# Performance work log

Hardware: AMD Instinct MI355X
Metric: run time of the kernel (lower is better)

The kernel has to match this reference:

```python
import jax, jax.numpy as jnp
import numpy as np

T, B, V, E = 256, 128, 256, 512
NN = (1024, 1024)  # num_nodes per LSTM layer


def setup_inputs() -> dict:
    key = jax.random.key(0)
    ks = jax.random.split(key, 8)
    inputs = jax.random.normal(ks[0], (T, B, V), jnp.float32)
    emb = jax.random.normal(ks[1], (V, E), jnp.float32) * np.float32(np.sqrt(1.0 / V))
    w0 = jax.random.normal(ks[2], (E + NN[0], 4 * NN[0]), jnp.float32) * np.float32(np.sqrt(1.0 / (E + NN[0])))
    b0 = jnp.zeros((4 * NN[0],), jnp.float32)
    w1 = jax.random.normal(ks[3], (NN[0] + NN[1], 4 * NN[1]), jnp.float32) * np.float32(np.sqrt(1.0 / (NN[0] + NN[1])))
    b1 = jnp.zeros((4 * NN[1],), jnp.float32)
    out_w = jax.random.normal(ks[4], (NN[1], V), jnp.float32) * np.float32(np.sqrt(1.0 / NN[1]))
    out_b = jnp.zeros((V,), jnp.float32)
    return {"inputs": inputs, "embedding_matrix": emb,
            "lstm_w0": w0, "lstm_b0": b0, "lstm_w1": w1, "lstm_b1": b1,
            "out_w": out_w, "out_b": out_b}


def reference(inputs, embedding_matrix, lstm_w0, lstm_b0, lstm_w1, lstm_b1, out_w, out_b):
    Tn, Bn, _ = inputs.shape
    # _embed: (stacked one-hot) @ embedding_matrix -> [T, B, E]
    embs = jnp.einsum('tbv,ve->tbe', inputs, embedding_matrix)
    ws = (lstm_w0, lstm_w1)
    bs = (lstm_b0, lstm_b1)
    init_states = tuple((jnp.zeros((Bn, n), embs.dtype), jnp.zeros((Bn, n), embs.dtype)) for n in NN)

    def step(states, emb):
        out = emb
        new_states = []
        for i in range(len(NN)):
            h, c = states[i]
            n = NN[i]
            # concat([dropout(inp), h]) @ W + b ; dropout_keep_prob = 1.0 -> identity
            lin = jnp.concatenate([out, h], axis=1) @ ws[i] + bs[i]
            f = jax.nn.sigmoid(lin[:, :n])
            ig = jax.nn.sigmoid(lin[:, n:2 * n])
            o = jax.nn.sigmoid(lin[:, 2 * n:3 * n])
            g = jnp.tanh(lin[:, 3 * n:])
            c = f * c + ig * g
            h = o * jnp.tanh(c)
            out = h
            new_states.append((h, c))
        return tuple(new_states), out

    _, rnn_outputs = jax.lax.scan(step, init_states, embs)  # [T, B, NN[-1]]
    # output module: concat over time (axis 0) then single dense layer
    hs = rnn_outputs.reshape(Tn * Bn, NN[-1])
    logits = hs @ out_w + out_b  # [T*B, V]
    return logits
```

## Files before the change

kernel.cpp:

```cpp
#include <hip/hip_runtime.h>
#include <hip/hip_bf16.h>
#include <cstdint>
#include <cstddef>

#define T_STEPS 256
#define BATCH   128
#define VOCAB   256
#define EDIM    512
#define NH      1024
#define GDIM    4096
#define NST0    40
#define NST1    64

typedef __attribute__((ext_vector_type(8))) short short8;
typedef __attribute__((ext_vector_type(4))) float floatx4;

__device__ __forceinline__ float sigmoidf_(float x) { return 1.0f / (1.0f + __expf(-x)); }
__device__ __forceinline__ float tanhf_(float x)    { return 1.0f - 2.0f / (__expf(2.0f * x) + 1.0f); }

typedef __attribute__((address_space(1))) const unsigned int guint;
typedef __attribute__((address_space(3))) unsigned int luint;
__device__ __forceinline__ void load_lds16(const void* g, void* l) {
    __builtin_amdgcn_global_load_lds((guint*)g, (luint*)l, 16, 0, 0);
}

#define BM 128
#define BN 128
#define BK 16
__global__ __launch_bounds__(256) void sgemm_f32(
    const float* __restrict__ A, const float* __restrict__ B,
    float* __restrict__ C, int M, int N, int K)
{
    __shared__ float As[BK][BM + 4];
    __shared__ float Bs[BK][BN + 4];
    const int tid = threadIdx.x;
    const int tr = tid >> 4, tc = tid & 15;
    const int bm = blockIdx.y, bn = blockIdx.x;
    const float* Ab = A + (size_t)bm * BM * K;
    float acc[8][8];
    #pragma unroll
    for (int i = 0; i < 8; ++i)
        #pragma unroll
        for (int j = 0; j < 8; ++j) acc[i][j] = 0.f;
    for (int k0 = 0; k0 < K; k0 += BK) {
        #pragma unroll
        for (int l = 0; l < 2; ++l) {
            int idx = tid + l * 256;
            int row = idx >> 2, c4 = idx & 3;
            float4 v = *(const float4*)(Ab + (size_t)row * K + k0 + c4 * 4);
            As[c4 * 4 + 0][row] = v.x; As[c4 * 4 + 1][row] = v.y;
            As[c4 * 4 + 2][row] = v.z; As[c4 * 4 + 3][row] = v.w;
        }
        #pragma unroll
        for (int l = 0; l < 2; ++l) {
            int idx = tid + l * 256;
            int row = idx >> 5, c4 = idx & 31;
            *(float4*)&Bs[row][c4 * 4] = *(const float4*)(B + (size_t)(k0 + row) * N + bn * BN + c4 * 4);
        }
        __syncthreads();
        #pragma unroll
        for (int kk = 0; kk < BK; ++kk) {
            float4 a0 = *(const float4*)&As[kk][tr * 8];
            float4 a1 = *(const float4*)&As[kk][tr * 8 + 4];
            float4 b0 = *(const float4*)&Bs[kk][tc * 8];
            float4 b1 = *(const float4*)&Bs[kk][tc * 8 + 4];
            float av[8] = {a0.x, a0.y, a0.z, a0.w, a1.x, a1.y, a1.z, a1.w};
            float bv[8] = {b0.x, b0.y, b0.z, b0.w, b1.x, b1.y, b1.z, b1.w};
            #pragma unroll
            for (int i = 0; i < 8; ++i)
                #pragma unroll
                for (int j = 0; j < 8; ++j) acc[i][j] += av[i] * bv[j];
        }
        __syncthreads();
    }
    #pragma unroll
    for (int i = 0; i < 8; ++i) {
        size_t row = (size_t)bm * BM + tr * 8 + i;
        #pragma unroll
        for (int j = 0; j < 8; j += 4) {
            int col = bn * BN + tc * 8 + j;
            *(float4*)(C + row * N + col) =
                make_float4(acc[i][j], acc[i][j+1], acc[i][j+2], acc[i][j+3]);
        }
    }
}

__global__ __launch_bounds__(256) void transpose_to_bf16(
    const float* __restrict__ src, __hip_bfloat16* __restrict__ dst, int R, int C)
{
    __shared__ float t[32][33];
    int x = blockIdx.x * 32 + threadIdx.x;
    #pragma unroll
    for (int i = 0; i < 4; ++i) {
        int y = blockIdx.y * 32 + threadIdx.y + i * 8;
        t[threadIdx.y + i * 8][threadIdx.x] = src[(size_t)y * C + x];
    }
    __syncthreads();
    int x2 = blockIdx.y * 32 + threadIdx.x;
    #pragma unroll
    for (int i = 0; i < 4; ++i) {
        int y2 = blockIdx.x * 32 + threadIdx.y + i * 8;
        dst[(size_t)y2 * R + x2] = __float2bfloat16(t[threadIdx.x][threadIdx.y + i * 8]);
    }
}

__global__ __launch_bounds__(256) void pack_w2(
    const float* __restrict__ src, __hip_bfloat16* __restrict__ dst,
    int koff, int NSTEPS)
{
    __shared__ float t[64][33];
    const int tid = threadIdx.x;
    const int xt = blockIdx.x;
    const int kt = blockIdx.y;
    {
        int yl = tid >> 3;
        int x0 = (tid & 7) * 8;
        const float* p = src + (size_t)(kt * 32 + yl) * GDIM + xt * 64 + x0;
        float4 v0 = *(const float4*)p;
        float4 v1 = *(const float4*)(p + 4);
        t[x0 + 0][yl] = v0.x; t[x0 + 1][yl] = v0.y; t[x0 + 2][yl] = v0.z; t[x0 + 3][yl] = v0.w;
        t[x0 + 4][yl] = v1.x; t[x0 + 5][yl] = v1.y; t[x0 + 6][yl] = v1.z; t[x0 + 7][yl] = v1.w;
    }
    __syncthreads();
    {
        int ll = tid >> 2;
        int quad = tid & 3;
        int lincol = xt * 64 + ll;
        int g = lincol >> 10, n = lincol & 1023;
        int j = n >> 3, c = n & 7;
        int tt = g >> 1;
        int l16 = (g & 1) * 8 + c;
        int s = (koff >> 5) + kt;
        __hip_bfloat16 o[8];
        #pragma unroll
        for (int jj = 0; jj < 8; ++jj)
            o[jj] = __float2bfloat16(t[ll][quad * 8 + jj]);
        size_t off = ((((size_t)j * NSTEPS + s) * 2 + tt) * 64 + (size_t)quad * 16 + l16) * 8;
        *(uint4*)(dst + off) = *(const uint4*)o;
    }
}

__global__ __launch_bounds__(256) void convert_to_bf16(
    const float* __restrict__ src, __hip_bfloat16* __restrict__ dst, size_t n4)
{
    size_t i = (size_t)blockIdx.x * 256 + threadIdx.x;
    if (i < n4) {
        float4 v = *(const float4*)(src + i * 4);
        __hip_bfloat16 o[4] = {__float2bfloat16(v.x), __float2bfloat16(v.y),
                               __float2bfloat16(v.z), __float2bfloat16(v.w)};
        *(uint2*)(dst + i * 4) = *(uint2*)o;
    }
}

#define GKP 40
__global__ __launch_bounds__(256) void gemm_bt(
    const __hip_bfloat16* __restrict__ A, const __hip_bfloat16* __restrict__ Bt,
    const float* __restrict__ bias, float* __restrict__ C, int M, int N, int K)
{
    __shared__ __hip_bfloat16 As[128 * GKP];
    __shared__ __hip_bfloat16 Bs[128 * GKP];
    const int tid = threadIdx.x;
    const int wave = tid >> 6, lane = tid & 63;
    const int quad = lane >> 4, l16 = lane & 15;
    const int wm = (wave >> 1) * 64, wn = (wave & 1) * 64;
    const size_t Arow0 = (size_t)blockIdx.y * 128;
    const size_t Brow0 = (size_t)blockIdx.x * 128;
    floatx4 acc[4][4];
    #pragma unroll
    for (int i = 0; i < 4; ++i)
        #pragma unroll
        for (int j = 0; j < 4; ++j) acc[i][j] = (floatx4)0.f;

    for (int k0 = 0; k0 < K; k0 += 32) {
        #pragma unroll
        for (int l = 0; l < 2; ++l) {
            int idx = tid + l * 256;
            int row = idx >> 2, seg = idx & 3;
            *(uint4*)(As + row * GKP + seg * 8) =
                *(const uint4*)(A + (Arow0 + row) * K + k0 + seg * 8);
            *(uint4*)(Bs + row * GKP + seg * 8) =
                *(const uint4*)(Bt + (Brow0 + row) * K + k0 + seg * 8);
        }
        __syncthreads();
        short8 af[4], bf[4];
        #pragma unroll
        for (int i = 0; i < 4; ++i)
            af[i] = *(const short8*)(As + (wm + i * 16 + l16) * GKP + quad * 8);
        #pragma unroll
        for (int j = 0; j < 4; ++j)
            bf[j] = *(const short8*)(Bs + (wn + j * 16 + l16) * GKP + quad * 8);
        #pragma unroll
        for (int i = 0; i < 4; ++i)
            #pragma unroll
            for (int j = 0; j < 4; ++j)
                acc[i][j] = __builtin_amdgcn_mfma_f32_16x16x32_bf16(af[i], bf[j], acc[i][j], 0, 0, 0);
        __syncthreads();
    }
    #pragma unroll
    for (int i = 0; i < 4; ++i)
        #pragma unroll
        for (int j = 0; j < 4; ++j) {
            int col = (int)Brow0 + wn + j * 16 + l16;
            float bv = bias ? bias[col] : 0.f;
            #pragma unroll
            for (int r = 0; r < 4; ++r) {
                size_t row = Arow0 + wm + i * 16 + quad * 4 + r;
                C[row * N + col] = acc[i][j][r] + bv;
            }
        }
}

template<int NC, int NCA0>
__device__ __forceinline__ void lstm_chunks(
    const __hip_bfloat16* __restrict__ pA0,
    const __hip_bfloat16* __restrict__ pA1,
    const __hip_bfloat16* Wlds, int lane,
    floatx4& acc0, floatx4& acc1)
{
    constexpr int D = 3;
    constexpr int P = (NC < D) ? NC : D;
    short8 af[D][8];
    #pragma unroll
    for (int c = 0; c < P; ++c) {
        const __hip_bfloat16* pa = (c < NCA0) ? (pA0 + (size_t)c * 256)
                                              : (pA1 + (size_t)(c - NCA0) * 256);
        #pragma unroll
        for (int ss = 0; ss < 8; ++ss)
            af[c % D][ss] = *(const short8*)(pa + ss * 32);
    }
    __syncthreads();
    #pragma unroll
    for (int c = 0; c < NC; ++c) {
        #pragma unroll
        for (int ss = 0; ss < 8; ++ss) {
            const int s = c * 8 + ss;
            short8 bf0 = *(const short8*)&Wlds[s * 1024 + lane * 8];
            short8 bf1 = *(const short8*)&Wlds[s * 1024 + 512 + lane * 8];
            acc0 = __builtin_amdgcn_mfma_f32_16x16x32_bf16(af[c % D][ss], bf0, acc0, 0, 0, 0);
            acc1 = __builtin_amdgcn_mfma_f32_16x16x32_bf16(af[c % D][ss], bf1, acc1, 0, 0, 0);
        }
        if (c + D < NC) {
            const int cn = c + D;
            const __hip_bfloat16* pa = (cn < NCA0) ? (pA0 + (size_t)cn * 256)
                                                   : (pA1 + (size_t)(cn - NCA0) * 256);
            #pragma unroll
            for (int ss = 0; ss < 8; ++ss)
                af[cn % D][ss] = *(const short8*)(pa + ss * 32);
        }
    }
}

__global__ __launch_bounds__(512) void lstm_diag(
    const __hip_bfloat16* __restrict__ inbf,
    const __hip_bfloat16* __restrict__ Wpack0,
    const __hip_bfloat16* __restrict__ Wpack1,
    const float* __restrict__ b0, const float* __restrict__ b1,
    __hip_bfloat16* __restrict__ h0_cur,
    const __hip_bfloat16* __restrict__ h0_prev,
    float* __restrict__ c0, float* __restrict__ c1,
    __hip_bfloat16* __restrict__ H1all,
    int d)
{
    const int bid = blockIdx.x;
    const int layer = (bid >> 3) & 1;
    const int j = ((bid >> 4) << 3) | (bid & 7);
    if (layer == 0 && d >= T_STEPS) return;
    if (layer == 1 && d == 0) return;

    __shared__ __attribute__((aligned(16))) __hip_bfloat16 Wlds[65536];

    const int tid = threadIdx.x;
    const int wave = tid >> 6, lane = tid & 63;
    const int quad = lane >> 4, l16 = lane & 15;

    const __hip_bfloat16 *A0, *A1;
    int A0stride;
    const float* bb; float* cst; __hip_bfloat16* hout;
    bool first;
    if (layer == 0) {
        first = (d == 0);
        bb = b0; cst = c0;
        A0 = inbf + (size_t)d * (BATCH * VOCAB); A0stride = VOCAB;
        A1 = h0_prev;
        hout = h0_cur;
        const __hip_bfloat16* Wp = Wpack0 + (size_t)j * (NST0 * 1024);
        #pragma unroll
        for (int it = 0; it < 10; ++it)
            load_lds16(Wp + it * 4096 + tid * 8, Wlds + it * 4096 + tid * 8);
    } else {
        first = (d == 1);
        bb = b1; cst = c1;
        A0 = h0_prev; A0stride = NH;
        A1 = (d >= 2) ? (H1all + (size_t)(d - 2) * (BATCH * NH)) : h0_prev;
        hout = H1all + (size_t)(d - 1) * (BATCH * NH);
        const __hip_bfloat16* Wp = Wpack1 + (size_t)j * (NST1 * 1024);
        #pragma unroll
        for (int it = 0; it < 16; ++it)
            load_lds16(Wp + it * 4096 + tid * 8, Wlds + it * 4096 + tid * 8);
    }

    const int row = wave * 16 + l16;
    const __hip_bfloat16* pA0 = A0 + (size_t)row * A0stride + quad * 8;
    const __hip_bfloat16* pA1 = A1 + (size_t)row * NH + quad * 8;

    const int cc = j * 8 + (l16 & 7);
    float bv0 = bb[((l16 < 8) ? 0 : 1) * NH + cc];
    float bv1 = bb[((l16 < 8) ? 2 : 3) * NH + cc];
    float cold[4];
    {
        const int bbase = 16 * wave + quad * 4;
        #pragma unroll
        for (int r = 0; r < 4; ++r)
            cold[r] = first ? 0.f : cst[(size_t)(bbase + r) * NH + cc];
    }
    floatx4 acc0 = {bv0, bv0, bv0, bv0};
    floatx4 acc1 = {bv1, bv1, bv1, bv1};

    if (layer == 0) {
        if (first) lstm_chunks<1, 1>(pA0, pA1, Wlds, lane, acc0, acc1);
        else       lstm_chunks<5, 1>(pA0, pA1, Wlds, lane, acc0, acc1);
    } else {
        if (first) lstm_chunks<4, 4>(pA0, pA1, Wlds, lane, acc0, acc1);
        else       lstm_chunks<8, 4>(pA0, pA1, Wlds, lane, acc0, acc1);
    }

    #pragma unroll
    for (int r = 0; r < 4; ++r) {
        float a0 = acc0[r], a1 = acc1[r];
        float p0 = __shfl_xor(a0, 8, 64);
        float p1 = __shfl_xor(a1, 8, 64);
        if (l16 < 8) {
            int b = 16 * wave + quad * 4 + r;
            float f  = sigmoidf_(a0);
            float ig = sigmoidf_(p0);
            float oo = sigmoidf_(a1);
            float gg = tanhf_(p1);
            size_t idx = (size_t)b * NH + cc;
            float cn = f * cold[r] + ig * gg;
            float hn = oo * tanhf_(cn);
            cst[idx] = cn;
            hout[idx] = __float2bfloat16(hn);
        }
    }
}

extern "C" void kernel_launch(void* const* d_in, const int* in_sizes, int n_in,
                              void* d_out, int out_size, void* d_ws, size_t ws_size,
                              hipStream_t stream)
{
    const float* inputs = (const float*)d_in[0];
    const float* emb    = (const float*)d_in[1];
    const float* w0     = (const float*)d_in[2];
    const float* b0     = (const float*)d_in[3];
    const float* w1     = (const float*)d_in[4];
    const float* b1     = (const float*)d_in[5];
    const float* outw   = (const float*)d_in[6];
    const float* outb   = (const float*)d_in[7];
    float* out = (float*)d_out;

    char* ws = (char*)d_ws;
    size_t off = 0;
    auto take = [&](size_t bytes) { char* p = ws + off; off += (bytes + 255) & ~(size_t)255; return p; };
    float* Wcomb = (float*)take((size_t)VOCAB * GDIM * 4);
    __hip_bfloat16* Wpack0 = (__hip_bfloat16*)take((size_t)128 * NST0 * 1024 * 2);
    __hip_bfloat16* Wpack1 = (__hip_bfloat16*)take((size_t)128 * NST1 * 1024 * 2);
    __hip_bfloat16* outwt  = (__hip_bfloat16*)take((size_t)NH * VOCAB * 2);
    __hip_bfloat16* inbf   = (__hip_bfloat16*)take((size_t)T_STEPS * BATCH * VOCAB * 2);
    __hip_bfloat16* h0pp0  = (__hip_bfloat16*)take((size_t)BATCH * NH * 2);
    __hip_bfloat16* h0pp1  = (__hip_bfloat16*)take((size_t)BATCH * NH * 2);
    float* c0 = (float*)take((size_t)BATCH * NH * 4);
    float* c1 = (float*)take((size_t)BATCH * NH * 4);
    __hip_bfloat16* H1all  = (__hip_bfloat16*)take((size_t)T_STEPS * BATCH * NH * 2);

    sgemm_f32<<<dim3(GDIM / BN, VOCAB / BM), 256, 0, stream>>>(
        emb, w0, Wcomb, VOCAB, GDIM, EDIM);
    pack_w2<<<dim3(64, VOCAB / 32), 256, 0, stream>>>(Wcomb, Wpack0, 0, NST0);
    pack_w2<<<dim3(64, NH / 32), 256, 0, stream>>>(w0 + (size_t)EDIM * GDIM, Wpack0, VOCAB, NST0);
    pack_w2<<<dim3(64, NH / 32), 256, 0, stream>>>(w1, Wpack1, 0, NST1);
    pack_w2<<<dim3(64, NH / 32), 256, 0, stream>>>(w1 + (size_t)NH * GDIM, Wpack1, NH, NST1);
    transpose_to_bf16<<<dim3(VOCAB / 32, NH / 32), dim3(32, 8), 0, stream>>>(
        outw, outwt, NH, VOCAB);
    {
        size_t n4 = (size_t)T_STEPS * BATCH * VOCAB / 4;
        convert_to_bf16<<<(int)((n4 + 255) / 256), 256, 0, stream>>>(inputs, inbf, n4);
    }

    for (int d = 0; d <= T_STEPS; ++d) {
        __hip_bfloat16* hcur = (d & 1) ? h0pp1 : h0pp0;
        __hip_bfloat16* hprev = (d & 1) ? h0pp0 : h0pp1;
        lstm_diag<<<256, 512, 0, stream>>>(
            inbf, Wpack0, Wpack1, b0, b1, hcur, hprev, c0, c1, H1all, d);
    }

    gemm_bt<<<dim3(VOCAB / 128, (T_STEPS * BATCH) / 128), 256, 0, stream>>>(
        H1all, outwt, outb, out, T_STEPS * BATCH, VOCAB, NH);
}
```

Measured before the change: 5.857 ms.

## Replace per-step LSTM launches with persistent cooperative kernel using grid barriers

Replaces the 257 per-diagonal kernel launches with one cooperative persistent kernel. It loads each block's packed weight slice into LDS once and keeps the cell state in registers. Steps are separated by an atomic-counter grid barrier, and the operand order is reordered so the shared h0 chunks are consumed with matching weight chunk offsets. This removes launch overhead, the repeated weight reloads into LDS and the cell-state global traffic. The cost is a grid-wide spin barrier per step and a dependence on all 256 blocks being co-resident, with a fallback to the old loop if the cooperative launch fails.

```diff
diff --git a/kernel.cpp b/kernel.cpp
--- a/kernel.cpp
+++ b/kernel.cpp
@@ -210,30 +210,30 @@
         }
 }
 
-template<int NC, int NCA0>
-__device__ __forceinline__ void lstm_chunks(
-    const __hip_bfloat16* __restrict__ pA0,
-    const __hip_bfloat16* __restrict__ pA1,
+template<int NCF, int NCS, int WF, int WS>
+__device__ __forceinline__ void chunks2(
+    const __hip_bfloat16* __restrict__ pF,
+    const __hip_bfloat16* __restrict__ pS,
     const __hip_bfloat16* Wlds, int lane,
     floatx4& acc0, floatx4& acc1)
 {
-    constexpr int D = 3;
-    constexpr int P = (NC < D) ? NC : D;
-    short8 af[D][8];
-    #pragma unroll
-    for (int c = 0; c < P; ++c) {
-        const __hip_bfloat16* pa = (c < NCA0) ? (pA0 + (size_t)c * 256)
-                                              : (pA1 + (size_t)(c - NCA0) * 256);
+    constexpr int NC = NCF + NCS;
+    constexpr int D = (NC < 3) ? NC : 3;
+    short8 af[3][8];
+    #pragma unroll
+    for (int c = 0; c < D; ++c) {
+        const __hip_bfloat16* pa = (c < NCF) ? (pF + (size_t)c * 256)
+                                             : (pS + (size_t)(c - NCF) * 256);
         #pragma unroll
         for (int ss = 0; ss < 8; ++ss)
             af[c % D][ss] = *(const short8*)(pa + ss * 32);
     }
-    __syncthreads();
     #pragma unroll
     for (int c = 0; c < NC; ++c) {
+        const int wc = (c < NCF) ? (WF + c) : (WS + (c - NCF));
         #pragma unroll
         for (int ss = 0; ss < 8; ++ss) {
-            const int s = c * 8 + ss;
+            const int s = wc * 8 + ss;
             short8 bf0 = *(const short8*)&Wlds[s * 1024 + lane * 8];
             short8 bf1 = *(const short8*)&Wlds[s * 1024 + 512 + lane * 8];
             acc0 = __builtin_amdgcn_mfma_f32_16x16x32_bf16(af[c % D][ss], bf0, acc0, 0, 0, 0);
@@ -241,8 +241,8 @@
         }
         if (c + D < NC) {
             const int cn = c + D;
-            const __hip_bfloat16* pa = (cn < NCA0) ? (pA0 + (size_t)cn * 256)
-                                                   : (pA1 + (size_t)(cn - NCA0) * 256);
+            const __hip_bfloat16* pa = (cn < NCF) ? (pF + (size_t)cn * 256)
+                                                  : (pS + (size_t)(cn - NCF) * 256);
             #pragma unroll
             for (int ss = 0; ss < 8; ++ss)
                 af[cn % D][ss] = *(const short8*)(pa + ss * 32);
@@ -316,12 +316,13 @@
     floatx4 acc0 = {bv0, bv0, bv0, bv0};
     floatx4 acc1 = {bv1, bv1, bv1, bv1};
 
+    __syncthreads();
     if (layer == 0) {
-        if (first) lstm_chunks<1, 1>(pA0, pA1, Wlds, lane, acc0, acc1);
-        else       lstm_chunks<5, 1>(pA0, pA1, Wlds, lane, acc0, acc1);
+        if (first) chunks2<1, 0, 0, 0>(pA0, pA0, Wlds, lane, acc0, acc1);
+        else       chunks2<1, 4, 0, 1>(pA0, pA1, Wlds, lane, acc0, acc1);
     } else {
-        if (first) lstm_chunks<4, 4>(pA0, pA1, Wlds, lane, acc0, acc1);
-        else       lstm_chunks<8, 4>(pA0, pA1, Wlds, lane, acc0, acc1);
+        if (first) chunks2<4, 0, 0, 0>(pA0, pA0, Wlds, lane, acc0, acc1);
+        else       chunks2<4, 4, 4, 0>(pA1, pA0, Wlds, lane, acc0, acc1);
     }
 
     #pragma unroll
@@ -344,6 +345,114 @@
     }
 }
 
+__device__ __forceinline__ void grid_barrier(uint32_t* cnt, uint32_t target) {
+    __syncthreads();
+    if (threadIdx.x == 0) {
+        __builtin_amdgcn_fence(__ATOMIC_RELEASE, "agent");
+        __hip_atomic_fetch_add(cnt, 1u, __ATOMIC_RELAXED, __HIP_MEMORY_SCOPE_AGENT);
+        while (__hip_atomic_load(cnt, __ATOMIC_RELAXED, __HIP_MEMORY_SCOPE_AGENT) < target)
+            __builtin_amdgcn_s_sleep(1);
+        __builtin_amdgcn_fence(__ATOMIC_ACQUIRE, "agent");
+    }
+    __syncthreads();
+}
+
+__global__ void zero_u32(uint32_t* p) { *p = 0; }
+
+__global__ __launch_bounds__(512) void lstm_persist2(
+    const __hip_bfloat16* __restrict__ inbf,
+    const __hip_bfloat16* __restrict__ Wpack0,
+    const __hip_bfloat16* __restrict__ Wpack1,
+    const float* __restrict__ b0, const float* __restrict__ b1,
+    __hip_bfloat16* __restrict__ h0pp0, __hip_bfloat16* __restrict__ h0pp1,
+    __hip_bfloat16* __restrict__ H1all,
+    uint32_t* __restrict__ bar)
+{
+    __shared__ __attribute__((aligned(16))) __hip_bfloat16 Wlds[65536];
+
+    const int bid = blockIdx.x;
+    const int layer = (bid >> 3) & 1;
+    const int j = ((bid >> 4) << 3) | (bid & 7);
+    const int tid = threadIdx.x;
+    const int wave = tid >> 6, lane = tid & 63;
+    const int quad = lane >> 4, l16 = lane & 15;
+
+    if (layer == 0) {
+        const __hip_bfloat16* Wp = Wpack0 + (size_t)j * (NST0 * 1024);
+        #pragma unroll
+        for (int it = 0; it < 10; ++it)
+            load_lds16(Wp + it * 4096 + tid * 8, Wlds + it * 4096 + tid * 8);
+    } else {
+        const __hip_bfloat16* Wp = Wpack1 + (size_t)j * (NST1 * 1024);
+        #pragma unroll
+        for (int it = 0; it < 16; ++it)
+            load_lds16(Wp + it * 4096 + tid * 8, Wlds + it * 4096 + tid * 8);
+    }
+    __syncthreads();
+
+    const int cc = j * 8 + (l16 & 7);
+    const float* bb = layer ? b1 : b0;
+    const float bv0 = bb[((l16 < 8) ? 0 : 1) * NH + cc];
+    const float bv1 = bb[((l16 < 8) ? 2 : 3) * NH + cc];
+    const int row = wave * 16 + l16;
+    float creg[4] = {0.f, 0.f, 0.f, 0.f};
+
+    for (int d = 0; d <= T_STEPS; ++d) {
+        if (d) grid_barrier(bar, (uint32_t)d * 256u);
+
+        const bool active = layer ? (d >= 1) : (d < T_STEPS);
+        if (!active) continue;
+
+        const __hip_bfloat16 *A0, *A1;
+        int A0stride;
+        bool first;
+        __hip_bfloat16* hout;
+        const __hip_bfloat16* h0_prev = (d & 1) ? h0pp0 : h0pp1;
+        if (layer == 0) {
+            first = (d == 0);
+            A0 = inbf + (size_t)d * (BATCH * VOCAB); A0stride = VOCAB;
+            A1 = h0_prev;
+            hout = (d & 1) ? h0pp1 : h0pp0;
+        } else {
+            first = (d == 1);
+            A0 = h0_prev; A0stride = NH;
+            A1 = (d >= 2) ? (H1all + (size_t)(d - 2) * (BATCH * NH)) : h0_prev;
+            hout = H1all + (size_t)(d - 1) * (BATCH * NH);
+        }
+
+        const __hip_bfloat16* pA0 = A0 + (size_t)row * A0stride + quad * 8;
+        const __hip_bfloat16* pA1 = A1 + (size_t)row * NH + quad * 8;
+        floatx4 acc0 = {bv0, bv0, bv0, bv0};
+        floatx4 acc1 = {bv1, bv1, bv1, bv1};
+
+        if (layer == 0) {
+            if (first) chunks2<1, 0, 0, 0>(pA0, pA0, Wlds, lane, acc0, acc1);
+            else       chunks2<1, 4, 0, 1>(pA0, pA1, Wlds, lane, acc0, acc1);
+        } else {
+            if (first) chunks2<4, 0, 0, 0>(pA0, pA0, Wlds, lane, acc0, acc1);
+            else       chunks2<4, 4, 4, 0>(pA1, pA0, Wlds, lane, acc0, acc1);
+        }
+
+        #pragma unroll
+        for (int r = 0; r < 4; ++r) {
+            float a0 = acc0[r], a1 = acc1[r];
+            float p0 = __shfl_xor(a0, 8, 64);
+            float p1 = __shfl_xor(a1, 8, 64);
+            if (l16 < 8) {
+                int b = 16 * wave + quad * 4 + r;
+                float f  = sigmoidf_(a0);
+                float ig = sigmoidf_(p0);
+                float oo = sigmoidf_(a1);
+                float gg = tanhf_(p1);
+                float cn = f * (first ? 0.f : creg[r]) + ig * gg;
+                creg[r] = cn;
+                float hn = oo * tanhf_(cn);
+                hout[(size_t)b * NH + cc] = __float2bfloat16(hn);
+            }
+        }
+    }
+}
+
 extern "C" void kernel_launch(void* const* d_in, const int* in_sizes, int n_in,
                               void* d_out, int out_size, void* d_ws, size_t ws_size,
                               hipStream_t stream)
@@ -370,6 +479,7 @@
     __hip_bfloat16* h0pp1  = (__hip_bfloat16*)take((size_t)BATCH * NH * 2);
     float* c0 = (float*)take((size_t)BATCH * NH * 4);
     float* c1 = (float*)take((size_t)BATCH * NH * 4);
+    uint32_t* bar = (uint32_t*)take(256);
     __hip_bfloat16* H1all  = (__hip_bfloat16*)take((size_t)T_STEPS * BATCH * NH * 2);
 
     sgemm_f32<<<dim3(GDIM / BN, VOCAB / BM), 256, 0, stream>>>(
@@ -384,12 +494,22 @@
         size_t n4 = (size_t)T_STEPS * BATCH * VOCAB / 4;
         convert_to_bf16<<<(int)((n4 + 255) / 256), 256, 0, stream>>>(inputs, inbf, n4);
     }
-
-    for (int d = 0; d <= T_STEPS; ++d) {
-        __hip_bfloat16* hcur = (d & 1) ? h0pp1 : h0pp0;
-        __hip_bfloat16* hprev = (d & 1) ? h0pp0 : h0pp1;
-        lstm_diag<<<256, 512, 0, stream>>>(
-            inbf, Wpack0, Wpack1, b0, b1, hcur, hprev, c0, c1, H1all, d);
+    zero_u32<<<1, 1, 0, stream>>>(bar);
+
+    {
+        void* args[] = { (void*)&inbf, (void*)&Wpack0, (void*)&Wpack1,
+                         (void*)&b0, (void*)&b1,
+                         (void*)&h0pp0, (void*)&h0pp1, (void*)&H1all, (void*)&bar };
+        hipError_t ce = hipLaunchCooperativeKernel(lstm_persist2, dim3(256), dim3(512),
+                                                   args, 0u, stream);
+        if (ce != hipSuccess) {
+            for (int d = 0; d <= T_STEPS; ++d) {
+                __hip_bfloat16* hcur = (d & 1) ? h0pp1 : h0pp0;
+                __hip_bfloat16* hprev = (d & 1) ? h0pp0 : h0pp1;
+                lstm_diag<<<256, 512, 0, stream>>>(
+                    inbf, Wpack0, Wpack1, b0, b1, hcur, hprev, c0, c1, H1all, d);
+            }
+        }
     }
 
     gemm_bt<<<dim3(VOCAB / 128, (T_STEPS * BATCH) / 128), 256, 0, stream>>>(
```

New measurement: 7.313 ms. 24.9% more time.
